# Performance work log

Measured on AMD Instinct MI355X. Metric: run time of the kernel, lower is better.

## Reference

```python
import jax, jax.numpy as jnp
import numpy as np

SCALE = 64 ** (-0.5)  # dim_head**-0.5; heads/dim_head otherwise unused in forward


def setup_inputs() -> dict:
    key = jax.random.key(0)
    ks = jax.random.split(key, 7)
    B, C, T = 8, 512, 4096
    s = C ** (-0.5)  # conv1d default init scale-ish
    x = jax.random.normal(ks[0], (B, C, T), dtype=jnp.float32)
    Wq = jax.random.normal(ks[1], (C, C), dtype=jnp.float32) * s
    bq = jax.random.normal(ks[2], (C,), dtype=jnp.float32) * s
    Wk = jax.random.normal(ks[3], (C, C), dtype=jnp.float32) * s
    bk = jax.random.normal(ks[4], (C,), dtype=jnp.float32) * s
    Wv = jax.random.normal(ks[5], (C, C), dtype=jnp.float32) * s
    bv = jax.random.normal(ks[6], (C,), dtype=jnp.float32) * s
    return {"x": x, "Wq": Wq, "bq": bq, "Wk": Wk, "bk": bk, "Wv": Wv, "bv": bv}


def reference(x, Wq, bq, Wk, bk, Wv, bv):
    # 1x1 Conv1d == per-timestep linear over channels: (o,c) x (b,c,t) -> (b,o,t)
    q = jnp.einsum('oc,bct->bot', Wq, x) + bq[None, :, None]
    k = jnp.einsum('oc,bct->bot', Wk, x) + bk[None, :, None]
    v = jnp.einsum('oc,bct->bot', Wv, x) + bv[None, :, None]
    # Channel-channel attention: dots (b, C, C); softmax over last (channel) axis
    dots = jnp.einsum('bct,bdt->bcd', q, k) * SCALE
    attn = jax.nn.softmax(dots, axis=-1)
    # (b,C,C) x (b,C,t) -> (b,C,t); dropout p=0 and to_out unused in original forward
    out = jnp.einsum('bcd,bdt->bct', attn, v)
    return out
```

## Files before the change

kernel.cpp:

```cpp
#include <hip/hip_runtime.h>

#define B_ 8
#define C_ 512
#define T_ 4096

typedef __attribute__((ext_vector_type(8))) __bf16 bf16x8;
typedef __attribute__((ext_vector_type(8))) _Float16 f16x8;
typedef __attribute__((ext_vector_type(8))) unsigned short u16x8;
typedef __attribute__((ext_vector_type(4))) float f32x4;

__device__ __forceinline__ unsigned short f2bf(float f) {
  unsigned int u = __float_as_uint(f);
  u += 0x7fffu + ((u >> 16) & 1u);
  return (unsigned short)(u >> 16);
}
__device__ __forceinline__ float bf2f(unsigned short h) {
  return __uint_as_float(((unsigned int)h) << 16);
}
__device__ __forceinline__ unsigned short f2h(float f) {
  return __builtin_bit_cast(unsigned short, (_Float16)f);
}

__device__ __forceinline__ void async16(unsigned short* ldsdst, const unsigned short* gsrc) {
  __builtin_amdgcn_global_load_lds(
      (__attribute__((address_space(1))) void*)(void*)const_cast<unsigned short*>(gsrc),
      (__attribute__((address_space(3))) void*)(void*)ldsdst,
      16, 0, 0);
}

template <bool F16>
__device__ __forceinline__ f32x4 mfma16(u16x8 a, u16x8 b, f32x4 c) {
  if constexpr (F16)
    return __builtin_amdgcn_mfma_f32_16x16x32_f16(
        __builtin_bit_cast(f16x8, a), __builtin_bit_cast(f16x8, b), c, 0, 0, 0);
  else
    return __builtin_amdgcn_mfma_f32_16x16x32_bf16(
        __builtin_bit_cast(bf16x8, a), __builtin_bit_cast(bf16x8, b), c, 0, 0, 0);
}

struct GemmP {
  const unsigned short* Ah; const unsigned short* Al; long sA; int lda;
  const unsigned short* Bh; const unsigned short* Bl; long sB; int ldb;
  float* Cf; unsigned short* Ch; unsigned short* Cl; long sC; int ldc;
  int kspan; int zparts;
  const float* rowv; const float* colv; const float* bq; const float* bk;
};

enum { EPI_F32 = 0, EPI_OUT = 1, EPI_DOTS = 2, EPI_SPLIT = 3, EPI_F16 = 4 };

template <int BM, int BN, int WM, int WN, bool SA, bool SB, int EPI, bool F16>
__global__ __launch_bounds__((BM / WM) * (BN / WN) * 64) void gemm_nt(GemmP g) {
  constexpr int KC = 64;
  constexpr int NWAVE = (BM / WM) * (BN / WN);
  constexpr int NT = NWAVE * 64;
  constexpr int ASZ = BM * KC, BSZ = BN * KC;
  constexpr int STAGE = (SA ? 2 : 1) * ASZ + (SB ? 2 : 1) * BSZ;
  constexpr int EPAD = BN + 4;
  constexpr int EPIB = 32 * EPAD * 4;
  constexpr int LDSB = (STAGE * 2 > EPIB) ? STAGE * 2 : EPIB;
  __shared__ alignas(16) char ldsraw[LDSB];
  unsigned short* lds = (unsigned short*)ldsraw;
  unsigned short* ldsAh = lds;
  unsigned short* ldsAl = lds + ASZ;
  unsigned short* ldsBh = lds + (SA ? 2 : 1) * ASZ;
  unsigned short* ldsBl = ldsBh + BSZ;

  const int tid = threadIdx.x;
  const int lane = tid & 63, wid = tid >> 6;
  constexpr int WNB = BN / WN;
  const int wm = wid / WNB, wn = wid % WNB;
  constexpr int MF = WM / 16, NF = WN / 16;

  const int bm = blockIdx.x, bn = blockIdx.y, z = blockIdx.z;
  const int b = z / g.zparts, kp = z - b * g.zparts;

  const unsigned short* Ah = g.Ah + (size_t)b * g.sA + (size_t)kp * g.kspan;
  const unsigned short* Al = SA ? (g.Al + (size_t)b * g.sA + (size_t)kp * g.kspan) : nullptr;
  const unsigned short* Bh = g.Bh + (size_t)b * g.sB + (size_t)kp * g.kspan;
  const unsigned short* Bl = SB ? (g.Bl + (size_t)b * g.sB + (size_t)kp * g.kspan) : nullptr;

  f32x4 acc[MF][NF] = {};

  const int kIters = g.kspan / KC;
  for (int kt = 0; kt < kIters; ++kt) {
    const int kb = kt * KC;
#pragma unroll
    for (int r = 0; r < ASZ / (8 * NT); ++r) {
      int idx = tid + r * NT;
      int row = idx >> 3, sl = idx & 7;
      int kc = (sl ^ (row & 7)) << 3;
      size_t goff = (size_t)(bm * BM + row) * g.lda + kb + kc;
      async16(&ldsAh[idx << 3], Ah + goff);
      if constexpr (SA) async16(&ldsAl[idx << 3], Al + goff);
    }
#pragma unroll
    for (int r = 0; r < BSZ / (8 * NT); ++r) {
      int idx = tid + r * NT;
      int row = idx >> 3, sl = idx & 7;
      int kc = (sl ^ (row & 7)) << 3;
      size_t goff = (size_t)(bn * BN + row) * g.ldb + kb + kc;
      async16(&ldsBh[idx << 3], Bh + goff);
      if constexpr (SB) async16(&ldsBl[idx << 3], Bl + goff);
    }
    __syncthreads();

    const int rsel = lane & 15, kq = lane >> 4;
#pragma unroll
    for (int ks = 0; ks < KC; ks += 32) {
      const int chunk = (ks >> 3) + kq;
      u16x8 afh[MF], afl[MF], bfh[NF], bfl[NF];
#pragma unroll
      for (int fm = 0; fm < MF; ++fm) {
        int row = wm * WM + fm * 16 + rsel;
        int ro = row * KC + ((chunk ^ (row & 7)) << 3);
        afh[fm] = *(const u16x8*)&ldsAh[ro];
        if constexpr (SA) afl[fm] = *(const u16x8*)&ldsAl[ro];
      }
#pragma unroll
      for (int fn = 0; fn < NF; ++fn) {
        int row = wn * WN + fn * 16 + rsel;
        int ro = row * KC + ((chunk ^ (row & 7)) << 3);
        bfh[fn] = *(const u16x8*)&ldsBh[ro];
        if constexpr (SB) bfl[fn] = *(const u16x8*)&ldsBl[ro];
      }
#pragma unroll
      for (int fm = 0; fm < MF; ++fm)
#pragma unroll
        for (int fn = 0; fn < NF; ++fn) {
          acc[fm][fn] = mfma16<F16>(afh[fm], bfh[fn], acc[fm][fn]);
          if constexpr (SB) acc[fm][fn] = mfma16<F16>(afh[fm], bfl[fn], acc[fm][fn]);
          if constexpr (SA) acc[fm][fn] = mfma16<F16>(afl[fm], bfh[fn], acc[fm][fn]);
        }
    }
    __syncthreads();
  }

  if constexpr (EPI == EPI_SPLIT || EPI == EPI_F16) {
#pragma unroll
    for (int fm = 0; fm < MF; ++fm)
#pragma unroll
      for (int fn = 0; fn < NF; ++fn)
#pragma unroll
        for (int r = 0; r < 4; ++r) {
          int i = bm * BM + wm * WM + fm * 16 + ((lane >> 4) << 2) + r;
          int j = bn * BN + wn * WN + fn * 16 + (lane & 15);
          float v = acc[fm][fn][r];
          size_t co = (size_t)z * g.sC + (size_t)i * g.ldc + j;
          if constexpr (EPI == EPI_SPLIT) {
            unsigned short h = f2bf(v);
            g.Ch[co] = h;
            g.Cl[co] = f2bf(v - bf2f(h));
          } else {
            g.Ch[co] = f2h(v);
          }
        }
  } else {
    float* eb = (float*)ldsraw;
#pragma unroll
    for (int ck = 0; ck < BM / 32; ++ck) {
      if (wm == ck) {
#pragma unroll
        for (int fi = 0; fi < MF; ++fi) {
#pragma unroll
          for (int fn = 0; fn < NF; ++fn)
#pragma unroll
            for (int r = 0; r < 4; ++r) {
              int lrow = fi * 16 + ((lane >> 4) << 2) + r;
              int col = wn * WN + fn * 16 + (lane & 15);
              eb[lrow * EPAD + col] = acc[fi][fn][r];
            }
        }
      }
      __syncthreads();
#pragma unroll
      for (int it = 0; it < (32 * BN / 4) / NT; ++it) {
        int idx = it * NT + tid;
        int row = idx / (BN / 4), c4 = (idx % (BN / 4)) * 4;
        f32x4 v = *(f32x4*)&eb[row * EPAD + c4];
        int grow = bm * BM + ck * 32 + row;
        int j = bn * BN + c4;
        if constexpr (EPI == EPI_OUT) v = v + g.rowv[b * C_ + grow];
        if constexpr (EPI == EPI_DOTS) {
          f32x4 bkv = *(const f32x4*)&g.bk[j];
          f32x4 ksv = *(const f32x4*)&g.colv[b * C_ + j];
          float qsi = g.rowv[b * C_ + grow], bqi = g.bq[grow];
          v = 0.125f * (v + qsi * bkv + bqi * (ksv + 4096.f * bkv));
        }
        *(f32x4*)&g.Cf[(size_t)z * g.sC + (size_t)grow * g.ldc + j] = v;
      }
      __syncthreads();
    }
  }
}

#define NXB (64 * 8 * 8)
#define PAD 66
__global__ __launch_bounds__(256) void prep_fused(
    const float* __restrict__ x, const float* __restrict__ Wq,
    const float* __restrict__ Wk, const float* __restrict__ Wv,
    unsigned short* __restrict__ Xh, unsigned short* __restrict__ XhT,
    float* __restrict__ S, unsigned short* Wqh, unsigned short* Wql,
    unsigned short* Wkh, unsigned short* Wkl, unsigned short* WvT) {
  __shared__ unsigned short tile[64 * PAD];
  const int tid = threadIdx.x;
  if (blockIdx.x < NXB) {
    const int tl = blockIdx.x;
    const int t0 = (tl & 63) << 6, c0 = ((tl >> 6) & 7) << 6, b = tl >> 9;
    const float* xin = x + ((size_t)(b * C_ + c0)) * T_ + t0;
    unsigned short* xo = Xh + ((size_t)(b * C_ + c0)) * T_ + t0;
#pragma unroll
    for (int r = 0; r < 4; ++r) {
      int p = tid + r * 256;
      int row = p >> 4, c4 = (p & 15) << 2;
      float4 v = *(const float4*)&xin[(size_t)row * T_ + c4];
      unsigned short h0 = f2h(v.x), h1 = f2h(v.y), h2 = f2h(v.z), h3 = f2h(v.w);
      ushort4 hv; hv.x = h0; hv.y = h1; hv.z = h2; hv.w = h3;
      *(ushort4*)&xo[(size_t)row * T_ + c4] = hv;
      unsigned int lo = (unsigned int)h0 | ((unsigned int)h1 << 16);
      unsigned int hi = (unsigned int)h2 | ((unsigned int)h3 << 16);
      ((unsigned int*)&tile[row * PAD + c4])[0] = lo;
      ((unsigned int*)&tile[row * PAD + c4])[1] = hi;
      float s = v.x + v.y + v.z + v.w;
#pragma unroll
      for (int o = 1; o < 16; o <<= 1) s += __shfl_xor(s, o);
      if ((tid & 15) == 0) atomicAdd(&S[b * C_ + c0 + row], s);
    }
    __syncthreads();
#pragma unroll
    for (int r = 0; r < 2; ++r) {
      int idx = tid + r * 256;
      int trow = idx >> 3, cc = (idx & 7) << 3;
      unsigned short vals[8];
#pragma unroll
      for (int j = 0; j < 8; ++j) vals[j] = tile[(cc + j) * PAD + trow];
      *(uint4*)&XhT[((size_t)b * T_ + t0 + trow) * C_ + c0 + cc] = *(uint4*)vals;
    }
  } else {
    int i = (blockIdx.x - NXB) * 256 + tid;
    float q = Wq[i]; unsigned short qh = f2bf(q); Wqh[i] = qh; Wql[i] = f2bf(q - bf2f(qh));
    float k = Wk[i]; unsigned short kh = f2bf(k); Wkh[i] = kh; Wkl[i] = f2bf(k - bf2f(kh));
    float v = Wv[i]; int d = i >> 9, e = i & 511;
    WvT[(e << 9) + d] = f2h(v);
  }
}

__global__ __launch_bounds__(256) void combine_g(const float* __restrict__ gp,
                                                 unsigned short* __restrict__ gh,
                                                 unsigned short* __restrict__ gl) {
  int i = blockIdx.x * 256 + threadIdx.x;
  int b = i >> 18, w = i & 0x3FFFF;
  const float* base = gp + ((size_t)b << 20);
  float v = base[w] + base[w + (1 << 18)] + base[w + 2 * (1 << 18)] + base[w + 3 * (1 << 18)];
  unsigned short h = f2bf(v);
  gh[i] = h;
  gl[i] = f2bf(v - bf2f(h));
}

__global__ __launch_bounds__(256) void qs_ks(const float* __restrict__ Wq, const float* __restrict__ Wk,
                                             const float* __restrict__ s, float* __restrict__ qs,
                                             float* __restrict__ ks) {
  int lane = threadIdx.x & 63, wid = threadIdx.x >> 6;
  int gi = blockIdx.x * 4 + wid;
  int b = gi >> 9, i = gi & 511;
  const float* sv = s + (b << 9);
  const float* wqr = Wq + (size_t)i * C_;
  const float* wkr = Wk + (size_t)i * C_;
  float aq = 0.f, ak = 0.f;
#pragma unroll
  for (int c = lane; c < C_; c += 64) {
    float sc = sv[c];
    aq += wqr[c] * sc;
    ak += wkr[c] * sc;
  }
#pragma unroll
  for (int o = 32; o > 0; o >>= 1) { aq += __shfl_down(aq, o); ak += __shfl_down(ak, o); }
  if (lane == 0) { qs[gi] = aq; ks[gi] = ak; }
}

__global__ __launch_bounds__(256) void softmax_rows(const float* __restrict__ logits,
                                                    const float* __restrict__ bv,
                                                    unsigned short* __restrict__ attn,
                                                    float* __restrict__ ab) {
  const int row = blockIdx.x;
  const int tid = threadIdx.x, lane = tid & 63, wid = tid >> 6;
  const float* L = logits + (size_t)row * C_;
  float v0 = L[tid], v1 = L[tid + 256];
  __shared__ float red[4];
  float m = fmaxf(v0, v1);
#pragma unroll
  for (int o = 32; o > 0; o >>= 1) m = fmaxf(m, __shfl_down(m, o));
  if (lane == 0) red[wid] = m;
  __syncthreads();
  m = fmaxf(fmaxf(red[0], red[1]), fmaxf(red[2], red[3]));
  __syncthreads();
  float e0 = __expf(v0 - m), e1 = __expf(v1 - m);
  float sum = e0 + e1;
#pragma unroll
  for (int o = 32; o > 0; o >>= 1) sum += __shfl_down(sum, o);
  if (lane == 0) red[wid] = sum;
  __syncthreads();
  sum = red[0] + red[1] + red[2] + red[3];
  float inv = 1.f / sum;
  float a0 = e0 * inv, a1 = e1 * inv;
  unsigned short* ar = attn + (size_t)row * C_;
  ar[tid] = f2h(a0);
  ar[tid + 256] = f2h(a1);
  float abv = a0 * bv[tid] + a1 * bv[tid + 256];
  __syncthreads();
#pragma unroll
  for (int o = 32; o > 0; o >>= 1) abv += __shfl_down(abv, o);
  if (lane == 0) red[wid] = abv;
  __syncthreads();
  if (tid == 0) ab[row] = red[0] + red[1] + red[2] + red[3];
}

extern "C" void kernel_launch(void* const* d_in, const int* in_sizes, int n_in,
                              void* d_out, int out_size, void* d_ws, size_t ws_size,
                              hipStream_t stream) {
  const float* x  = (const float*)d_in[0];
  const float* Wq = (const float*)d_in[1];
  const float* bq = (const float*)d_in[2];
  const float* Wk = (const float*)d_in[3];
  const float* bk = (const float*)d_in[4];
  const float* Wv = (const float*)d_in[5];
  const float* bv = (const float*)d_in[6];
  float* out = (float*)d_out;

  char* ws = (char*)d_ws;
  size_t off = 0;
  auto alloc = [&](size_t bytes) {
    char* p = ws + off;
    off += (bytes + 255) & ~(size_t)255;
    return p;
  };
  const size_t XSZ = (size_t)B_ * C_ * T_;
  const size_t GSZ = (size_t)B_ * C_ * C_;

  unsigned short* Xh  = (unsigned short*)alloc(XSZ * 2);
  unsigned short* XhT = (unsigned short*)alloc(XSZ * 2);
  float* Gpart = (float*)alloc((size_t)4 * GSZ * 4);
  unsigned short* Gh = (unsigned short*)alloc(GSZ * 2);
  unsigned short* Gl = (unsigned short*)alloc(GSZ * 2);
  unsigned short* Ph = (unsigned short*)alloc(GSZ * 2);
  unsigned short* Pl = (unsigned short*)alloc(GSZ * 2);
  float* Logits = (float*)alloc(GSZ * 4);
  unsigned short* Attn = (unsigned short*)alloc(GSZ * 2);
  unsigned short* Mh = (unsigned short*)alloc(GSZ * 2);
  unsigned short* Wqh = (unsigned short*)alloc((size_t)C_ * C_ * 2);
  unsigned short* Wql = (unsigned short*)alloc((size_t)C_ * C_ * 2);
  unsigned short* Wkh = (unsigned short*)alloc((size_t)C_ * C_ * 2);
  unsigned short* Wkl = (unsigned short*)alloc((size_t)C_ * C_ * 2);
  unsigned short* WvT = (unsigned short*)alloc((size_t)C_ * C_ * 2);
  float* S  = (float*)alloc((size_t)B_ * C_ * 4);
  float* Qs = (float*)alloc((size_t)B_ * C_ * 4);
  float* Ks = (float*)alloc((size_t)B_ * C_ * 4);
  float* Ab = (float*)alloc((size_t)B_ * C_ * 4);

  hipMemsetAsync(S, 0, (size_t)B_ * C_ * 4, stream);
  prep_fused<<<NXB + C_ * C_ / 256, 256, 0, stream>>>(x, Wq, Wk, Wv, Xh, XhT, S,
                                                      Wqh, Wql, Wkh, Wkl, WvT);
  qs_ks<<<B_ * C_ / 4, 256, 0, stream>>>(Wq, Wk, S, Qs, Ks);

  {
    GemmP p = {};
    p.Ah = Xh; p.sA = (long)C_ * T_; p.lda = T_;
    p.Bh = Xh; p.sB = (long)C_ * T_; p.ldb = T_;
    p.Cf = Gpart; p.sC = (long)C_ * C_; p.ldc = C_;
    p.kspan = T_ / 4; p.zparts = 4;
    gemm_nt<128, 128, 32, 64, false, false, EPI_F32, true>
        <<<dim3(4, 4, 32), 512, 0, stream>>>(p);
  }
  combine_g<<<(int)(GSZ / 256), 256, 0, stream>>>(Gpart, Gh, Gl);

  {
    GemmP p = {};
    p.Ah = Wqh; p.Al = Wql; p.sA = 0; p.lda = C_;
    p.Bh = Gh; p.Bl = Gl; p.sB = (long)C_ * C_; p.ldb = C_;
    p.Ch = Ph; p.Cl = Pl; p.sC = (long)C_ * C_; p.ldc = C_;
    p.kspan = C_; p.zparts = 1;
    gemm_nt<64, 64, 32, 32, true, true, EPI_SPLIT, false>
        <<<dim3(8, 8, 8), 256, 0, stream>>>(p);
  }
  {
    GemmP p = {};
    p.Ah = Ph; p.Al = Pl; p.sA = (long)C_ * C_; p.lda = C_;
    p.Bh = Wkh; p.Bl = Wkl; p.sB = 0; p.ldb = C_;
    p.Cf = Logits; p.sC = (long)C_ * C_; p.ldc = C_;
    p.kspan = C_; p.zparts = 1;
    p.rowv = Qs; p.colv = Ks; p.bq = bq; p.bk = bk;
    gemm_nt<64, 64, 32, 32, true, true, EPI_DOTS, false>
        <<<dim3(8, 8, 8), 256, 0, stream>>>(p);
  }
  softmax_rows<<<B_ * C_, 256, 0, stream>>>(Logits, bv, Attn, Ab);
  {
    GemmP p = {};
    p.Ah = Attn; p.sA = (long)C_ * C_; p.lda = C_;
    p.Bh = WvT; p.sB = 0; p.ldb = C_;
    p.Ch = Mh; p.sC = (long)C_ * C_; p.ldc = C_;
    p.kspan = C_; p.zparts = 1;
    gemm_nt<64, 64, 32, 32, false, false, EPI_F16, true>
        <<<dim3(8, 8, 8), 256, 0, stream>>>(p);
  }
  {
    GemmP p = {};
    p.Ah = Mh; p.sA = (long)C_ * C_; p.lda = C_;
    p.Bh = XhT; p.sB = (long)C_ * T_; p.ldb = C_;
    p.Cf = out; p.sC = (long)C_ * T_; p.ldc = T_;
    p.kspan = C_; p.zparts = 1;
    p.rowv = Ab;
    gemm_nt<128, 128, 32, 64, false, false, EPI_OUT, true>
        <<<dim3(C_ / 128, T_ / 128, B_), 512, 0, stream>>>(p);
  }
  (void)in_sizes; (void)n_in; (void)out_size; (void)ws_size;
}
```

Baseline: 255.9 us.

## Exploit Gram symmetry: compute lower-triangle tiles, mirror in combine, retile output GEMM

The X·Xᵀ Gram GEMM now launches only the 10 lower-triangular 128x128 tiles per batch and uses 8 K-splits instead of 4. The combine kernel sums the 8 partials per 64x64 tile and transposes through shared memory to fill the mirrored upper tiles. This cuts the Gram work nearly in half. Separately, the final output GEMM switches to 64x64 warp tiles with 256 threads, which needed an epilogue fix for multi-fragment warp rows. The tradeoffs are larger partial buffers, extra partial-sum traffic, and more registers per thread in the output GEMM.

Result: no change. 255.1 us (-0.3%).

```diff
diff --git a/kernel.cpp b/kernel.cpp
--- a/kernel.cpp
+++ b/kernel.cpp
@@ -48,7 +48,7 @@
 
 enum { EPI_F32 = 0, EPI_OUT = 1, EPI_DOTS = 2, EPI_SPLIT = 3, EPI_F16 = 4 };
 
-template <int BM, int BN, int WM, int WN, bool SA, bool SB, int EPI, bool F16>
+template <int BM, int BN, int WM, int WN, bool SA, bool SB, int EPI, bool F16, bool TRI>
 __global__ __launch_bounds__((BM / WM) * (BN / WN) * 64) void gemm_nt(GemmP g) {
   constexpr int KC = 64;
   constexpr int NWAVE = (BM / WM) * (BN / WN);
@@ -71,7 +71,15 @@
   const int wm = wid / WNB, wn = wid % WNB;
   constexpr int MF = WM / 16, NF = WN / 16;
 
-  const int bm = blockIdx.x, bn = blockIdx.y, z = blockIdx.z;
+  int bm, bn;
+  if constexpr (TRI) {
+    const int t = blockIdx.x;
+    const int tm = (t >= 6) ? 3 : (t >= 3) ? 2 : (t >= 1) ? 1 : 0;
+    bm = tm; bn = t - (tm * (tm + 1)) / 2;
+  } else {
+    bm = blockIdx.x; bn = blockIdx.y;
+  }
+  const int z = blockIdx.z;
   const int b = z / g.zparts, kp = z - b * g.zparts;
 
   const unsigned short* Ah = g.Ah + (size_t)b * g.sA + (size_t)kp * g.kspan;
@@ -158,16 +166,18 @@
     float* eb = (float*)ldsraw;
 #pragma unroll
     for (int ck = 0; ck < BM / 32; ++ck) {
-      if (wm == ck) {
-#pragma unroll
-        for (int fi = 0; fi < MF; ++fi) {
+      if (wm == (ck * 32) / WM) {
+        const int fm0 = ((ck * 32) % WM) / 16;
+#pragma unroll
+        for (int fi = 0; fi < 2; ++fi) {
+          int fm = fm0 + fi;
 #pragma unroll
           for (int fn = 0; fn < NF; ++fn)
 #pragma unroll
             for (int r = 0; r < 4; ++r) {
               int lrow = fi * 16 + ((lane >> 4) << 2) + r;
               int col = wn * WN + fn * 16 + (lane & 15);
-              eb[lrow * EPAD + col] = acc[fi][fn][r];
+              eb[lrow * EPAD + col] = acc[fm][fn][r];
             }
         }
       }
@@ -247,13 +257,51 @@
 __global__ __launch_bounds__(256) void combine_g(const float* __restrict__ gp,
                                                  unsigned short* __restrict__ gh,
                                                  unsigned short* __restrict__ gl) {
-  int i = blockIdx.x * 256 + threadIdx.x;
-  int b = i >> 18, w = i & 0x3FFFF;
-  const float* base = gp + ((size_t)b << 20);
-  float v = base[w] + base[w + (1 << 18)] + base[w + 2 * (1 << 18)] + base[w + 3 * (1 << 18)];
-  unsigned short h = f2bf(v);
-  gh[i] = h;
-  gl[i] = f2bf(v - bf2f(h));
+  __shared__ float tile[64 * 65];
+  const int blk = blockIdx.x;
+  const int b = blk >> 6, tr = (blk >> 3) & 7, tc = blk & 7;
+  const bool mirror = (tr >> 1) < (tc >> 1);
+  const int sr = mirror ? tc : tr, sc = mirror ? tr : tc;
+  const float* src = gp + ((size_t)b << 21) + (size_t)(sr << 6) * 512 + (sc << 6);
+  const int row = threadIdx.x >> 4, c4 = (threadIdx.x & 15) << 2;
+  float vals[4][4];
+#pragma unroll
+  for (int rr = 0; rr < 4; ++rr) {
+    const int r = row + rr * 16;
+    f32x4 v = {};
+#pragma unroll
+    for (int p = 0; p < 8; ++p)
+      v += *(const f32x4*)&src[((size_t)p << 18) + (size_t)r * 512 + c4];
+    if (mirror) {
+#pragma unroll
+      for (int k = 0; k < 4; ++k) tile[r * 65 + c4 + k] = v[k];
+    } else {
+#pragma unroll
+      for (int k = 0; k < 4; ++k) vals[rr][k] = v[k];
+    }
+  }
+  if (mirror) {
+    __syncthreads();
+#pragma unroll
+    for (int rr = 0; rr < 4; ++rr) {
+      const int r = row + rr * 16;
+#pragma unroll
+      for (int k = 0; k < 4; ++k) vals[rr][k] = tile[(c4 + k) * 65 + r];
+    }
+  }
+  unsigned short* ghp = gh + ((size_t)b << 18) + (size_t)(tr << 6) * 512 + (tc << 6);
+  unsigned short* glp = gl + ((size_t)b << 18) + (size_t)(tr << 6) * 512 + (tc << 6);
+#pragma unroll
+  for (int rr = 0; rr < 4; ++rr) {
+    const int r = row + rr * 16;
+    ushort4 h, l;
+    h.x = f2bf(vals[rr][0]); l.x = f2bf(vals[rr][0] - bf2f(h.x));
+    h.y = f2bf(vals[rr][1]); l.y = f2bf(vals[rr][1] - bf2f(h.y));
+    h.z = f2bf(vals[rr][2]); l.z = f2bf(vals[rr][2] - bf2f(h.z));
+    h.w = f2bf(vals[rr][3]); l.w = f2bf(vals[rr][3] - bf2f(h.w));
+    *(ushort4*)&ghp[(size_t)r * 512 + c4] = h;
+    *(ushort4*)&glp[(size_t)r * 512 + c4] = l;
+  }
 }
 
 __global__ __launch_bounds__(256) void qs_ks(const float* __restrict__ Wq, const float* __restrict__ Wk,
@@ -338,7 +386,7 @@
 
   unsigned short* Xh  = (unsigned short*)alloc(XSZ * 2);
   unsigned short* XhT = (unsigned short*)alloc(XSZ * 2);
-  float* Gpart = (float*)alloc((size_t)4 * GSZ * 4);
+  float* Gpart = (float*)alloc((size_t)8 * GSZ * 4);
   unsigned short* Gh = (unsigned short*)alloc(GSZ * 2);
   unsigned short* Gl = (unsigned short*)alloc(GSZ * 2);
   unsigned short* Ph = (unsigned short*)alloc(GSZ * 2);
@@ -366,11 +414,11 @@
     p.Ah = Xh; p.sA = (long)C_ * T_; p.lda = T_;
     p.Bh = Xh; p.sB = (long)C_ * T_; p.ldb = T_;
     p.Cf = Gpart; p.sC = (long)C_ * C_; p.ldc = C_;
-    p.kspan = T_ / 4; p.zparts = 4;
-    gemm_nt<128, 128, 32, 64, false, false, EPI_F32, true>
-        <<<dim3(4, 4, 32), 512, 0, stream>>>(p);
-  }
-  combine_g<<<(int)(GSZ / 256), 256, 0, stream>>>(Gpart, Gh, Gl);
+    p.kspan = T_ / 8; p.zparts = 8;
+    gemm_nt<128, 128, 32, 64, false, false, EPI_F32, true, true>
+        <<<dim3(10, 1, 64), 512, 0, stream>>>(p);
+  }
+  combine_g<<<B_ * 64, 256, 0, stream>>>(Gpart, Gh, Gl);
 
   {
     GemmP p = {};
@@ -378,7 +426,7 @@
     p.Bh = Gh; p.Bl = Gl; p.sB = (long)C_ * C_; p.ldb = C_;
     p.Ch = Ph; p.Cl = Pl; p.sC = (long)C_ * C_; p.ldc = C_;
     p.kspan = C_; p.zparts = 1;
-    gemm_nt<64, 64, 32, 32, true, true, EPI_SPLIT, false>
+    gemm_nt<64, 64, 32, 32, true, true, EPI_SPLIT, false, false>
         <<<dim3(8, 8, 8), 256, 0, stream>>>(p);
   }
   {
@@ -388,7 +436,7 @@
     p.Cf = Logits; p.sC = (long)C_ * C_; p.ldc = C_;
     p.kspan = C_; p.zparts = 1;
     p.rowv = Qs; p.colv = Ks; p.bq = bq; p.bk = bk;
-    gemm_nt<64, 64, 32, 32, true, true, EPI_DOTS, false>
+    gemm_nt<64, 64, 32, 32, true, true, EPI_DOTS, false, false>
         <<<dim3(8, 8, 8), 256, 0, stream>>>(p);
   }
   softmax_rows<<<B_ * C_, 256, 0, stream>>>(Logits, bv, Attn, Ab);
@@ -398,7 +446,7 @@
     p.Bh = WvT; p.sB = 0; p.ldb = C_;
     p.Ch = Mh; p.sC = (long)C_ * C_; p.ldc = C_;
     p.kspan = C_; p.zparts = 1;
-    gemm_nt<64, 64, 32, 32, false, false, EPI_F16, true>
+    gemm_nt<64, 64, 32, 32, false, false, EPI_F16, true, false>
         <<<dim3(8, 8, 8), 256, 0, stream>>>(p);
   }
   {
@@ -408,8 +456,8 @@
     p.Cf = out; p.sC = (long)C_ * T_; p.ldc = T_;
     p.kspan = C_; p.zparts = 1;
     p.rowv = Ab;
-    gemm_nt<128, 128, 32, 64, false, false, EPI_OUT, true>
-        <<<dim3(C_ / 128, T_ / 128, B_), 512, 0, stream>>>(p);
+    gemm_nt<128, 128, 64, 64, false, false, EPI_OUT, true, false>
+        <<<dim3(C_ / 128, T_ / 128, B_), 256, 0, stream>>>(p);
   }
   (void)in_sizes; (void)n_in; (void)out_size; (void)ws_size;
 }
```
